# Performance work log

Hardware: AMD Instinct MI355X
Metric: run time of the kernel (lower is better)

The kernel has to match this reference:

```python
import jax, jax.numpy as jnp
import numpy as np

B, S, E = 4, 2048, 768
DFF = 4 * E
EPS = 1e-5


def _layernorm(x, g, b):
    mu = jnp.mean(x, axis=-1, keepdims=True)
    var = jnp.mean(jnp.square(x - mu), axis=-1, keepdims=True)
    return (x - mu) * jax.lax.rsqrt(var + EPS) * g + b


def setup_inputs() -> dict:
    key = jax.random.key(0)
    ks = jax.random.split(key, 16)
    w = lambda k, shp: jax.random.normal(k, shp, dtype=jnp.float32) * 0.02
    inp = {
        "x": jax.random.normal(ks[0], (B, S, E), dtype=jnp.float32),
        "kv": jax.random.normal(ks[1], (B, S, E), dtype=jnp.float32),
        "wq_w": w(ks[2], (E, E)), "wq_b": jnp.zeros((E,), jnp.float32),
        "wk_w": w(ks[3], (E, E)), "wk_b": jnp.zeros((E,), jnp.float32),
        "wv_w": w(ks[4], (E, E)), "wv_b": jnp.zeros((E,), jnp.float32),
        "ln1_g": jnp.ones((E,), jnp.float32), "ln1_b": jnp.zeros((E,), jnp.float32),
        "wq2_w": w(ks[5], (E, E)), "wq2_b": jnp.zeros((E,), jnp.float32),
        "wk2_w": w(ks[6], (E, E)), "wk2_b": jnp.zeros((E,), jnp.float32),
        "wv2_w": w(ks[7], (E, E)), "wv2_b": jnp.zeros((E,), jnp.float32),
        "ln2_g": jnp.ones((E,), jnp.float32), "ln2_b": jnp.zeros((E,), jnp.float32),
        "w1": w(ks[8], (DFF, E)), "b1": jnp.zeros((DFF,), jnp.float32),
        "w2": w(ks[9], (E, DFF)), "b2": jnp.zeros((E,), jnp.float32),
        "ln3_g": jnp.ones((E,), jnp.float32), "ln3_b": jnp.zeros((E,), jnp.float32),
    }
    return inp


def reference(x, kv, wq_w, wq_b, wk_w, wk_b, wv_w, wv_b, ln1_g, ln1_b,
              wq2_w, wq2_b, wk2_w, wk2_b, wv2_w, wv2_b, ln2_g, ln2_b,
              w1, b1, w2, b2, ln3_g, ln3_b):
    scalar = 1.0 / np.sqrt(E).astype(np.float32)
    mask_value = jnp.finfo(x.dtype).min
    s = x.shape[1]
    causal = jnp.triu(jnp.ones((s, s), dtype=bool), k=1)  # True above diagonal -> masked

    # ---- causal self-attention (single head, full E) ----
    q = x @ wq_w.T + wq_b
    k = x @ wk_w.T + wk_b
    v = x @ wv_w.T + wv_b
    scores = jnp.einsum('bqe,bke->bqk', q, k) * scalar
    scores = jnp.where(causal, mask_value, scores)
    h1 = jnp.einsum('bqk,bke->bqe', jax.nn.softmax(scores, axis=-1), v)
    x = _layernorm(x + h1, ln1_g, ln1_b)

    # ---- cross-attention over kv (no mask) ----
    q2 = x @ wq2_w.T + wq2_b
    k2 = kv @ wk2_w.T + wk2_b
    v2 = kv @ wv2_w.T + wv2_b
    scores2 = jnp.einsum('bqe,bke->bqk', q2, k2) * scalar
    h2 = jnp.einsum('bqk,bke->bqe', jax.nn.softmax(scores2, axis=-1), v2)
    x = _layernorm(x + h2, ln2_g, ln2_b)

    # ---- MLP: Linear -> ReLU -> Linear -> ReLU (note trailing ReLU) ----
    h = jax.nn.relu(x @ w1.T + b1)
    mlp = jax.nn.relu(h @ w2.T + b2)
    return _layernorm(x + mlp, ln3_g, ln3_b)
```

## Files before the change

kernel.cpp:

```cpp
#include <hip/hip_runtime.h>
#include <hip/hip_bf16.h>
#include <math.h>


typedef __bf16 bf16_t;
typedef bf16_t bf16x8 __attribute__((ext_vector_type(8)));
typedef float f32x4 __attribute__((ext_vector_type(4)));

struct MMDesc {
    const bf16_t* A;
    const bf16_t* B;
    const float* bias;
    __hip_bfloat16* C;
    float* lsum;
    int koff;
    int trans;
};
struct MMArgs { MMDesc g[8]; };

__device__ __forceinline__ void load16(const bf16_t* g, bf16_t* l) {
    __builtin_amdgcn_global_load_lds(
        (const __attribute__((address_space(1))) unsigned int*)g,
        (__attribute__((address_space(3))) unsigned int*)l, 16, 0, 0);
}

__device__ __forceinline__ void rd4(const bf16_t* p, int s0, int s1, bf16x8 f[4][2]) {
#pragma unroll
    for (int i = 0; i < 4; ++i) {
        f[i][0] = *(const bf16x8*)(p + i * 1024 + s0);
        f[i][1] = *(const bf16x8*)(p + i * 1024 + s1);
    }
}
__device__ __forceinline__ void rd2(const bf16_t* p, int s0, int s1, bf16x8 f[2][2]) {
#pragma unroll
    for (int i = 0; i < 2; ++i) {
        f[i][0] = *(const bf16x8*)(p + i * 1024 + s0);
        f[i][1] = *(const bf16x8*)(p + i * 1024 + s1);
    }
}

#define SBAR asm volatile("s_barrier" ::: "memory")
#define SCH  __builtin_amdgcn_sched_barrier(0)
#define MID  do { SCH; SBAR; SCH; __builtin_amdgcn_s_setprio(1); } while (0)
#define END0 do { __builtin_amdgcn_s_setprio(0); SCH; \
    asm volatile("s_waitcnt lgkmcnt(0)" ::: "memory"); SBAR; SCH; } while (0)
#define ENDV do { __builtin_amdgcn_s_setprio(0); SCH; \
    asm volatile("s_waitcnt vmcnt(4) lgkmcnt(0)" ::: "memory"); SBAR; SCH; } while (0)

#define QMFMA(mh, nh, BF) do { \
    _Pragma("unroll") \
    for (int ks = 0; ks < 2; ++ks) \
    _Pragma("unroll") \
    for (int mi = 0; mi < 4; ++mi) \
    _Pragma("unroll") \
    for (int ni = 0; ni < 2; ++ni) \
        acc[(mh) * 4 + mi][(nh) * 2 + ni] = __builtin_amdgcn_mfma_f32_16x16x32_bf16( \
            af[mi][ks], BF[ni][ks], acc[(mh) * 4 + mi][(nh) * 2 + ni], 0, 0, 0); \
} while (0)

__device__ __forceinline__ void mm8_core(
    const bf16_t* Ag, const bf16_t* Bg, int lda, int ldb, int K,
    bf16_t* lds, int w, int l, f32x4 acc[8][4])
{
    const long ldal = lda, ldbl = ldb;
    const int fr = l & 15, kq = l >> 4;
    const int rr = w * 8 + (l >> 3);
    const int c8e = ((l & 7) ^ (l >> 3)) * 8;
    const bf16_t* As = Ag + (long)rr * ldal + c8e;
    const bf16_t* Bs = Bg + (long)rr * ldbl + c8e;
    const int s0 = ((0 + kq) ^ (fr & 7)) * 8;
    const int s1 = ((4 + kq) ^ (fr & 7)) * 8;
    const bf16_t* lA = lds + ((w >> 2) * 64 + fr) * 64;
    const bf16_t* lB = lds + 16384 + ((w & 3) * 32 + fr) * 64;
    bf16_t* stA = lds + w * 512;
    bf16_t* stB = lds + 16384 + w * 512;

    auto stg = [&](int b, int isB, int h, int t) {
        const long ld = isB ? ldbl : ldal;
        const bf16_t* g = (isB ? Bs : As) + (long)h * 128 * ld + (long)t * 64;
        bf16_t* d = (isB ? stB : stA) + b * 32768 + h * 8192;
        load16(g, d);
        load16(g + 64 * ld, d + 4096);
    };

    bf16x8 af[4][2], bf0[2][2], bf1[2][2];
    const int NT = K >> 6, NI = NT >> 1;

    stg(0, 0, 0, 0); stg(0, 1, 0, 0); stg(0, 1, 1, 0); stg(0, 0, 1, 0);
    stg(1, 0, 0, 1); stg(1, 1, 0, 1);
    asm volatile("s_waitcnt vmcnt(4)" ::: "memory");
    SBAR; SCH;

    for (int i = 0; i < NI; ++i) {
        const int t1 = 2 * i + 1;
        int t2 = 2 * i + 2; if (t2 >= NT) t2 -= 2;
        int t3 = 2 * i + 3; if (t3 >= NT) t3 -= 2;
        rd4(lA, s0, s1, af); rd2(lB, s0, s1, bf0);
        stg(1, 1, 1, t1);
        MID; QMFMA(0, 0, bf0); END0;
        rd2(lB + 8192, s0, s1, bf1);
        stg(1, 0, 1, t1);
        MID; QMFMA(0, 1, bf1); END0;
        rd4(lA + 8192, s0, s1, af);
        stg(0, 0, 0, t2);
        MID; QMFMA(1, 0, bf0); END0;
        stg(0, 1, 0, t2);
        MID; QMFMA(1, 1, bf1); ENDV;
        rd4(lA + 32768, s0, s1, af); rd2(lB + 32768, s0, s1, bf0);
        stg(0, 1, 1, t2);
        MID; QMFMA(0, 0, bf0); END0;
        rd2(lB + 32768 + 8192, s0, s1, bf1);
        stg(0, 0, 1, t2);
        MID; QMFMA(0, 1, bf1); END0;
        rd4(lA + 32768 + 8192, s0, s1, af);
        stg(1, 0, 0, t3);
        MID; QMFMA(1, 0, bf0); END0;
        stg(1, 1, 0, t3);
        MID; QMFMA(1, 1, bf1); ENDV;
    }
    asm volatile("s_waitcnt vmcnt(0)" ::: "memory");
    SBAR; SCH;
}

template <bool RELU, bool CLAMPK>
__global__ __launch_bounds__(512, 2) void mm8_std(
    MMArgs args, int M, int N, int K, int lda, int ldb, float scale, int GX)
{
    __shared__ __align__(16) bf16_t lds[65536];
    const MMDesc dsc = args.g[blockIdx.z];

    const int lin = blockIdx.x;
    const int panel = lin / (8 * GX);
    const int rem = lin - panel * 8 * GX;
    const int bx = rem >> 3;
    const int by = panel * 8 + (rem & 7);
    const int m0 = by * 256, n0 = bx * 256;
    const int tid = threadIdx.x, w = tid >> 6, l = tid & 63;

    f32x4 acc[8][4];
    const f32x4 z4 = {0.f, 0.f, 0.f, 0.f};
#pragma unroll
    for (int i = 0; i < 8; ++i)
#pragma unroll
        for (int j = 0; j < 4; ++j) acc[i][j] = z4;

    int Keff = K;
    if (CLAMPK) {
        int km = (by + 1) * 256 - dsc.koff;
        Keff = km < K ? km : K;
    }
    if (!CLAMPK || Keff > 0)
        mm8_core(dsc.A + (long)m0 * lda, dsc.B + (long)n0 * ldb,
                 lda, ldb, Keff, lds, w, l, acc);

    const int fr = l & 15, erow = (l >> 4) * 4;
    const int wrow = (w >> 2) * 64, wcol = (w & 3) * 32;
    __hip_bfloat16* ct = (__hip_bfloat16*)lds;
#pragma unroll
    for (int mh = 0; mh < 2; ++mh) {
        if (mh) __syncthreads();
#pragma unroll
        for (int nh = 0; nh < 2; ++nh)
#pragma unroll
            for (int ni = 0; ni < 2; ++ni) {
                const int cl = nh * 128 + wcol + ni * 16 + fr;
                const float bv = dsc.bias ? dsc.bias[n0 + cl] : 0.f;
#pragma unroll
                for (int mi = 0; mi < 4; ++mi) {
                    const int lr = wrow + mi * 16 + erow;
                    const f32x4 a = acc[mh * 4 + mi][nh * 2 + ni];
#pragma unroll
                    for (int r = 0; r < 4; ++r) {
                        float v = a[r] * scale + bv;
                        if (RELU) v = fmaxf(v, 0.f);
                        ct[dsc.trans ? (cl * 136 + lr + r) : ((lr + r) * 264 + cl)]
                            = __float2bfloat16(v);
                    }
                }
            }
        __syncthreads();
        if (dsc.trans) {
            __hip_bfloat16* base = dsc.C + ((long)(m0 >> 11) * N + n0) * 2048
                                 + (m0 & 2047) + mh * 128;
#pragma unroll
            for (int u = 0; u < 8; ++u) {
                const int e = u * 4096 + tid * 8;
                *(uint4*)(base + (long)(e >> 7) * 2048 + (e & 127))
                    = *(const uint4*)(ct + (e >> 7) * 136 + (e & 127));
            }
        } else {
            __hip_bfloat16* base = dsc.C + (long)(m0 + mh * 128) * N + n0;
#pragma unroll
            for (int u = 0; u < 8; ++u) {
                const int e = u * 4096 + tid * 8;
                *(uint4*)(base + (long)(e >> 8) * N + (e & 255))
                    = *(const uint4*)(ct + (e >> 8) * 264 + (e & 255));
            }
        }
    }
}

template <bool CAUSAL>
__global__ __launch_bounds__(512, 2) void mm8_exp(
    MMArgs args, int N, int K, int lda, int ldb, float scale, int GX)
{
    __shared__ __align__(16) bf16_t lds[65536];
    const MMDesc dsc = args.g[blockIdx.z];

    int bx, by;
    if (CAUSAL) {
        const int t = blockIdx.x;
        by = (int)((sqrtf(8.f * t + 1.f) - 1.f) * 0.5f);
        while ((by + 1) * (by + 2) / 2 <= t) ++by;
        while (by * (by + 1) / 2 > t) --by;
        bx = t - by * (by + 1) / 2;
    } else {
        const int lin = blockIdx.x;
        const int panel = lin / (8 * GX);
        const int rem = lin - panel * 8 * GX;
        bx = rem >> 3;
        by = panel * 8 + (rem & 7);
    }
    const int m0 = by * 256, n0 = bx * 256;
    const int tid = threadIdx.x, w = tid >> 6, l = tid & 63;

    f32x4 acc[8][4];
    const f32x4 z4 = {0.f, 0.f, 0.f, 0.f};
#pragma unroll
    for (int i = 0; i < 8; ++i)
#pragma unroll
        for (int j = 0; j < 4; ++j) acc[i][j] = z4;

    mm8_core(dsc.A + (long)m0 * lda, dsc.B + (long)n0 * ldb,
             lda, ldb, K, lds, w, l, acc);

    const int fr = l & 15, erow = (l >> 4) * 4;
    const int wrow = (w >> 2) * 64, wcol = (w & 3) * 32;
    __hip_bfloat16* ct = (__hip_bfloat16*)lds;
#pragma unroll
    for (int mh = 0; mh < 2; ++mh) {
        if (mh) __syncthreads();
#pragma unroll
        for (int mi = 0; mi < 4; ++mi) {
            const int lr = wrow + mi * 16 + erow;
#pragma unroll
            for (int r = 0; r < 4; ++r) {
                const int grow = m0 + mh * 128 + lr + r;
                float rs = 0.f;
#pragma unroll
                for (int nh = 0; nh < 2; ++nh)
#pragma unroll
                    for (int ni = 0; ni < 2; ++ni) {
                        const int cl = nh * 128 + wcol + ni * 16 + fr;
                        float e;
                        if (CAUSAL && (n0 + cl) > grow)
                            e = 0.f;
                        else
                            e = __expf(acc[mh * 4 + mi][nh * 2 + ni][r] * scale);
                        ct[(lr + r) * 264 + cl] = __float2bfloat16(e);
                        rs += e;
                    }
#pragma unroll
                for (int o = 8; o > 0; o >>= 1) rs += __shfl_down(rs, o, 16);
                if ((l & 15) == 0) atomicAdd(&dsc.lsum[grow], rs);
            }
        }
        __syncthreads();
        __hip_bfloat16* base = dsc.C + (long)(m0 + mh * 128) * N + n0;
#pragma unroll
        for (int u = 0; u < 8; ++u) {
            const int e = u * 4096 + tid * 8;
            *(uint4*)(base + (long)(e >> 8) * N + (e & 255))
                = *(const uint4*)(ct + (e >> 8) * 264 + (e & 255));
        }
    }
}

__device__ __forceinline__ float waveReduceSum(float v) {
#pragma unroll
    for (int o = 32; o > 0; o >>= 1) v += __shfl_down(v, o, 64);
    return v;
}
__device__ __forceinline__ float blockReduceSum(float v, float* s) {
    int lane = threadIdx.x & 63, w = threadIdx.x >> 6;
    v = waveReduceSum(v);
    __syncthreads();
    if (lane == 0) s[w] = v;
    __syncthreads();
    return s[0] + s[1] + s[2] + s[3];
}

template <bool BR, bool XF32>
__global__ __launch_bounds__(256) void ln_kernel(
    const float* __restrict__ xf, const __hip_bfloat16* __restrict__ xh,
    const __hip_bfloat16* __restrict__ h1, const __hip_bfloat16* __restrict__ h2,
    const float* __restrict__ hbias, const float* __restrict__ lsum,
    const float* __restrict__ g, const float* __restrict__ beta,
    float* __restrict__ outf, __hip_bfloat16* __restrict__ outb) {
    __shared__ float red[4];
    const int E = 768;
    const long row = blockIdx.x;
    const float hscale = lsum ? (1.f / lsum[row]) : 1.f;

    float vals[3];
    float sum = 0.f;
#pragma unroll
    for (int i = 0; i < 3; ++i) {
        int c = threadIdx.x + i * 256;
        float t = __bfloat162float(h1[row * E + c]) + __bfloat162float(h2[row * E + c]);
        if (BR) t = fmaxf(t + hbias[c], 0.f);
        else t *= hscale;
        float xv = XF32 ? xf[row * E + c] : __bfloat162float(xh[row * E + c]);
        vals[i] = xv + t;
        sum += vals[i];
    }
    sum = blockReduceSum(sum, red);
    const float mean = sum * (1.f / 768.f);

    float ss = 0.f;
#pragma unroll
    for (int i = 0; i < 3; ++i) {
        float d = vals[i] - mean;
        ss += d * d;
    }
    ss = blockReduceSum(ss, red);
    const float inv = rsqrtf(ss * (1.f / 768.f) + 1e-5f);

#pragma unroll
    for (int i = 0; i < 3; ++i) {
        int c = threadIdx.x + i * 256;
        float v = (vals[i] - mean) * inv * g[c] + beta[c];
        if (outf) outf[row * E + c] = v;
        if (outb) outb[row * E + c] = __float2bfloat16(v);
    }
}

struct CvtPtrs {
    const float* s[10];
    __hip_bfloat16* d[10];
};
__global__ __launch_bounds__(256) void cvt_all(CvtPtrs p) {
    int bid = blockIdx.x, seg, off;
    if (bid < 3456) {
        seg = bid / 576;
        off = (bid % 576) * 1024;
    } else if (bid < 8064) {
        int t = bid - 3456;
        seg = 6 + t / 2304;
        off = (t % 2304) * 1024;
    } else {
        int t = bid - 8064;
        seg = 8 + t / 6144;
        off = (t % 6144) * 1024;
    }
    const float* s = p.s[seg];
    __hip_bfloat16* d = p.d[seg];
    int i = off + threadIdx.x * 4;
    float4 v = *(const float4*)(s + i);
    d[i + 0] = __float2bfloat16(v.x);
    d[i + 1] = __float2bfloat16(v.y);
    d[i + 2] = __float2bfloat16(v.z);
    d[i + 3] = __float2bfloat16(v.w);
}

extern "C" void kernel_launch(void* const* d_in, const int* in_sizes, int n_in,
                              void* d_out, int out_size, void* d_ws, size_t ws_size,
                              hipStream_t stream) {
    const int Bb = 4, S = 2048, E = 768, DFF = 3072;
    const int Nr = Bb * S;

    const float* x    = (const float*)d_in[0];
    const float* kv   = (const float*)d_in[1];
    const float* wq_w = (const float*)d_in[2];
    const float* wq_b = (const float*)d_in[3];
    const float* wk_w = (const float*)d_in[4];
    const float* wk_b = (const float*)d_in[5];
    const float* wv_w = (const float*)d_in[6];
    const float* wv_b = (const float*)d_in[7];
    const float* ln1g = (const float*)d_in[8];
    const float* ln1b = (const float*)d_in[9];
    const float* wq2w = (const float*)d_in[10];
    const float* wq2b = (const float*)d_in[11];
    const float* wk2w = (const float*)d_in[12];
    const float* wk2b = (const float*)d_in[13];
    const float* wv2w = (const float*)d_in[14];
    const float* wv2b = (const float*)d_in[15];
    const float* ln2g = (const float*)d_in[16];
    const float* ln2b = (const float*)d_in[17];
    const float* w1   = (const float*)d_in[18];
    const float* b1   = (const float*)d_in[19];
    const float* w2   = (const float*)d_in[20];
    const float* b2   = (const float*)d_in[21];
    const float* ln3g = (const float*)d_in[22];
    const float* ln3b = (const float*)d_in[23];
    float* out = (float*)d_out;

    char* wsp = (char*)d_ws;
    auto alloc = [&](size_t bytes) {
        char* p = wsp;
        wsp += (bytes + 255) & ~(size_t)255;
        return p;
    };
    const size_t nSE = (size_t)Nr * E;
    const size_t nSS = (size_t)Bb * S * S;
    __hip_bfloat16* Pb   = (__hip_bfloat16*)alloc(nSS * 2);
    __hip_bfloat16* qb   = (__hip_bfloat16*)alloc(nSE * 2);
    __hip_bfloat16* kb   = (__hip_bfloat16*)alloc(nSE * 2);
    __hip_bfloat16* hffb = Pb;
    __hip_bfloat16* vtb  = (__hip_bfloat16*)alloc(nSE * 2);
    __hip_bfloat16* xb   = (__hip_bfloat16*)alloc(nSE * 2);
    __hip_bfloat16* kvb  = (__hip_bfloat16*)alloc(nSE * 2);
    __hip_bfloat16* actb = (__hip_bfloat16*)alloc(nSE * 2);
    __hip_bfloat16* hA   = (__hip_bfloat16*)alloc(nSE * 2);
    __hip_bfloat16* hB   = (__hip_bfloat16*)alloc(nSE * 2);
    __hip_bfloat16* wqb   = (__hip_bfloat16*)alloc((size_t)E * E * 2);
    __hip_bfloat16* wkb   = (__hip_bfloat16*)alloc((size_t)E * E * 2);
    __hip_bfloat16* wvb   = (__hip_bfloat16*)alloc((size_t)E * E * 2);
    __hip_bfloat16* wq2bm = (__hip_bfloat16*)alloc((size_t)E * E * 2);
    __hip_bfloat16* wk2bm = (__hip_bfloat16*)alloc((size_t)E * E * 2);
    __hip_bfloat16* wv2bm = (__hip_bfloat16*)alloc((size_t)E * E * 2);
    __hip_bfloat16* w1b   = (__hip_bfloat16*)alloc((size_t)DFF * E * 2);
    __hip_bfloat16* w2b   = (__hip_bfloat16*)alloc((size_t)E * DFF * 2);
    float* lsum1 = (float*)alloc((size_t)Nr * 4);
    float* lsum2 = (float*)alloc((size_t)Nr * 4);

    const float scale = 1.0f / sqrtf((float)E);
    const dim3 blk(256);
    const dim3 blk5(512);

    hipMemsetAsync(lsum1, 0, (size_t)Nr * 4 * 2, stream);

    CvtPtrs cp;
    cp.s[0] = wq_w; cp.d[0] = wqb;
    cp.s[1] = wk_w; cp.d[1] = wkb;
    cp.s[2] = wv_w; cp.d[2] = wvb;
    cp.s[3] = wq2w; cp.d[3] = wq2bm;
    cp.s[4] = wk2w; cp.d[4] = wk2bm;
    cp.s[5] = wv2w; cp.d[5] = wv2bm;
    cp.s[6] = w1;   cp.d[6] = w1b;
    cp.s[7] = w2;   cp.d[7] = w2b;
    cp.s[8] = x;    cp.d[8] = xb;
    cp.s[9] = kv;   cp.d[9] = kvb;
    cvt_all<<<8064 + 12288, blk, 0, stream>>>(cp);

    {
        MMArgs a{};
        a.g[0] = {(const bf16_t*)xb, (const bf16_t*)wqb, wq_b, qb, nullptr, 0, 0};
        a.g[1] = {(const bf16_t*)xb, (const bf16_t*)wkb, wk_b, kb, nullptr, 0, 0};
        a.g[2] = {(const bf16_t*)xb, (const bf16_t*)wvb, wv_b, vtb, nullptr, 0, 1};
        mm8_std<false, false><<<dim3(96, 1, 3), blk5, 0, stream>>>(
            a, Nr, E, E, E, E, 1.f, 3);
    }
    {
        MMArgs a{};
        for (int b = 0; b < 4; ++b)
            a.g[b] = {(const bf16_t*)qb + (long)b * S * E,
                      (const bf16_t*)kb + (long)b * S * E, nullptr,
                      Pb + (long)b * S * S, lsum1 + b * S, 0, 0};
        mm8_exp<true><<<dim3(36, 1, 4), blk5, 0, stream>>>(a, S, E, E, E, scale, 8);
    }
    {
        MMArgs a{};
        for (int b = 0; b < 4; ++b)
            for (int ks = 0; ks < 2; ++ks)
                a.g[b * 2 + ks] = {(const bf16_t*)Pb + (long)b * S * S + ks * 1024,
                                   (const bf16_t*)vtb + (long)b * E * S + ks * 1024,
                                   nullptr, (ks ? hB : hA) + (long)b * S * E,
                                   nullptr, ks * 1024, 0};
        mm8_std<false, true><<<dim3(24, 1, 8), blk5, 0, stream>>>(
            a, S, E, 1024, S, S, 1.f, 3);
    }
    ln_kernel<false, true><<<Nr, blk, 0, stream>>>(
        x, nullptr, hA, hB, nullptr, lsum1, ln1g, ln1b, nullptr, actb);

    {
        MMArgs a{};
        a.g[0] = {(const bf16_t*)actb, (const bf16_t*)wq2bm, wq2b, qb, nullptr, 0, 0};
        a.g[1] = {(const bf16_t*)kvb, (const bf16_t*)wk2bm, wk2b, kb, nullptr, 0, 0};
        a.g[2] = {(const bf16_t*)kvb, (const bf16_t*)wv2bm, wv2b, vtb, nullptr, 0, 1};
        mm8_std<false, false><<<dim3(96, 1, 3), blk5, 0, stream>>>(
            a, Nr, E, E, E, E, 1.f, 3);
    }
    {
        MMArgs a{};
        for (int b = 0; b < 4; ++b)
            a.g[b] = {(const bf16_t*)qb + (long)b * S * E,
                      (const bf16_t*)kb + (long)b * S * E, nullptr,
                      Pb + (long)b * S * S, lsum2 + b * S, 0, 0};
        mm8_exp<false><<<dim3(64, 1, 4), blk5, 0, stream>>>(a, S, E, E, E, scale, 8);
    }
    {
        MMArgs a{};
        for (int b = 0; b < 4; ++b)
            for (int ks = 0; ks < 2; ++ks)
                a.g[b * 2 + ks] = {(const bf16_t*)Pb + (long)b * S * S + ks * 1024,
                                   (const bf16_t*)vtb + (long)b * E * S + ks * 1024,
                                   nullptr, (ks ? hB : hA) + (long)b * S * E,
                                   nullptr, 0, 0};
        mm8_std<false, false><<<dim3(24, 1, 8), blk5, 0, stream>>>(
            a, S, E, 1024, S, S, 1.f, 3);
    }
    ln_kernel<false, false><<<Nr, blk, 0, stream>>>(
        nullptr, actb, hA, hB, nullptr, lsum2, ln2g, ln2b, nullptr, actb);

    {
        MMArgs a{};
        a.g[0] = {(const bf16_t*)actb, (const bf16_t*)w1b, b1, hffb, nullptr, 0, 0};
        mm8_std<true, false><<<dim3(384, 1, 1), blk5, 0, stream>>>(
            a, Nr, DFF, E, E, E, 1.f, 12);
    }
    {
        MMArgs a{};
        a.g[0] = {(const bf16_t*)hffb, (const bf16_t*)w2b, nullptr, hA, nullptr, 0, 0};
        a.g[1] = {(const bf16_t*)hffb + 1536, (const bf16_t*)w2b + 1536, nullptr,
                  hB, nullptr, 0, 0};
        mm8_std<false, false><<<dim3(96, 1, 2), blk5, 0, stream>>>(
            a, Nr, E, 1536, DFF, DFF, 1.f, 3);
    }
    ln_kernel<true, false><<<Nr, blk, 0, stream>>>(
        nullptr, actb, hA, hB, b2, nullptr, ln3g, ln3b, out, nullptr);
}
```

Baseline: 542.7 us.

## Hoist cross-attn K/V projections into first projection launch and relax GEMM waits

The cross-attention K2/V2 projections depend only on kv, so they move into the first batched projection launch (z=5), and the later launch computes only Q2. This fills the GPU better and removes work from the serial chain. K2/V2 are staged in the output buffer as scratch, which is safe only if d_out is large enough and is overwritten afterwards. Separately, the GEMM main loop drops the per-phase lgkmcnt(0) wait plus trailing barrier, keeping a single barrier before each MFMA block and an explicit vmcnt(4) wait. This relies on the remaining barriers and the compiler's own waits to keep LDS reads correct.

```diff
diff --git a/kernel.cpp b/kernel.cpp
--- a/kernel.cpp
+++ b/kernel.cpp
@@ -41,11 +41,10 @@
 
 #define SBAR asm volatile("s_barrier" ::: "memory")
 #define SCH  __builtin_amdgcn_sched_barrier(0)
-#define MID  do { SCH; SBAR; SCH; __builtin_amdgcn_s_setprio(1); } while (0)
-#define END0 do { __builtin_amdgcn_s_setprio(0); SCH; \
-    asm volatile("s_waitcnt lgkmcnt(0)" ::: "memory"); SBAR; SCH; } while (0)
-#define ENDV do { __builtin_amdgcn_s_setprio(0); SCH; \
-    asm volatile("s_waitcnt vmcnt(4) lgkmcnt(0)" ::: "memory"); SBAR; SCH; } while (0)
+#define PBAR do { SCH; SBAR; SCH; } while (0)
+#define PRIO1 __builtin_amdgcn_s_setprio(1)
+#define PRIO0 __builtin_amdgcn_s_setprio(0)
+#define VMC4 asm volatile("s_waitcnt vmcnt(4)" ::: "memory")
 
 #define QMFMA(mh, nh, BF) do { \
     _Pragma("unroll") \
@@ -97,26 +96,28 @@
         int t3 = 2 * i + 3; if (t3 >= NT) t3 -= 2;
         rd4(lA, s0, s1, af); rd2(lB, s0, s1, bf0);
         stg(1, 1, 1, t1);
-        MID; QMFMA(0, 0, bf0); END0;
+        PBAR; PRIO1; QMFMA(0, 0, bf0); PRIO0;
         rd2(lB + 8192, s0, s1, bf1);
         stg(1, 0, 1, t1);
-        MID; QMFMA(0, 1, bf1); END0;
+        PBAR; PRIO1; QMFMA(0, 1, bf1); PRIO0;
         rd4(lA + 8192, s0, s1, af);
         stg(0, 0, 0, t2);
-        MID; QMFMA(1, 0, bf0); END0;
+        PBAR; PRIO1; QMFMA(1, 0, bf0); PRIO0;
         stg(0, 1, 0, t2);
-        MID; QMFMA(1, 1, bf1); ENDV;
+        VMC4;
+        PBAR; PRIO1; QMFMA(1, 1, bf1); PRIO0;
         rd4(lA + 32768, s0, s1, af); rd2(lB + 32768, s0, s1, bf0);
         stg(0, 1, 1, t2);
-        MID; QMFMA(0, 0, bf0); END0;
+        PBAR; PRIO1; QMFMA(0, 0, bf0); PRIO0;
         rd2(lB + 32768 + 8192, s0, s1, bf1);
         stg(0, 0, 1, t2);
-        MID; QMFMA(0, 1, bf1); END0;
+        PBAR; PRIO1; QMFMA(0, 1, bf1); PRIO0;
         rd4(lA + 32768 + 8192, s0, s1, af);
         stg(1, 0, 0, t3);
-        MID; QMFMA(1, 0, bf0); END0;
+        PBAR; PRIO1; QMFMA(1, 0, bf0); PRIO0;
         stg(1, 1, 0, t3);
-        MID; QMFMA(1, 1, bf1); ENDV;
+        VMC4;
+        PBAR; PRIO1; QMFMA(1, 1, bf1); PRIO0;
     }
     asm volatile("s_waitcnt vmcnt(0)" ::: "memory");
     SBAR; SCH;
@@ -424,6 +425,9 @@
     float* lsum1 = (float*)alloc((size_t)Nr * 4);
     float* lsum2 = (float*)alloc((size_t)Nr * 4);
 
+    __hip_bfloat16* k2b  = (__hip_bfloat16*)d_out;
+    __hip_bfloat16* vtb2 = k2b + nSE;
+
     const float scale = 1.0f / sqrtf((float)E);
     const dim3 blk(256);
     const dim3 blk5(512);
@@ -445,10 +449,12 @@
 
     {
         MMArgs a{};
-        a.g[0] = {(const bf16_t*)xb, (const bf16_t*)wqb, wq_b, qb, nullptr, 0, 0};
-        a.g[1] = {(const bf16_t*)xb, (const bf16_t*)wkb, wk_b, kb, nullptr, 0, 0};
-        a.g[2] = {(const bf16_t*)xb, (const bf16_t*)wvb, wv_b, vtb, nullptr, 0, 1};
-        mm8_std<false, false><<<dim3(96, 1, 3), blk5, 0, stream>>>(
+        a.g[0] = {(const bf16_t*)xb,  (const bf16_t*)wqb,   wq_b, qb,   nullptr, 0, 0};
+        a.g[1] = {(const bf16_t*)xb,  (const bf16_t*)wkb,   wk_b, kb,   nullptr, 0, 0};
+        a.g[2] = {(const bf16_t*)xb,  (const bf16_t*)wvb,   wv_b, vtb,  nullptr, 0, 1};
+        a.g[3] = {(const bf16_t*)kvb, (const bf16_t*)wk2bm, wk2b, k2b,  nullptr, 0, 0};
+        a.g[4] = {(const bf16_t*)kvb, (const bf16_t*)wv2bm, wv2b, vtb2, nullptr, 0, 1};
+        mm8_std<false, false><<<dim3(96, 1, 5), blk5, 0, stream>>>(
             a, Nr, E, E, E, E, 1.f, 3);
     }
     {
@@ -476,16 +482,14 @@
     {
         MMArgs a{};
         a.g[0] = {(const bf16_t*)actb, (const bf16_t*)wq2bm, wq2b, qb, nullptr, 0, 0};
-        a.g[1] = {(const bf16_t*)kvb, (const bf16_t*)wk2bm, wk2b, kb, nullptr, 0, 0};
-        a.g[2] = {(const bf16_t*)kvb, (const bf16_t*)wv2bm, wv2b, vtb, nullptr, 0, 1};
-        mm8_std<false, false><<<dim3(96, 1, 3), blk5, 0, stream>>>(
+        mm8_std<false, false><<<dim3(96, 1, 1), blk5, 0, stream>>>(
             a, Nr, E, E, E, E, 1.f, 3);
     }
     {
         MMArgs a{};
         for (int b = 0; b < 4; ++b)
             a.g[b] = {(const bf16_t*)qb + (long)b * S * E,
-                      (const bf16_t*)kb + (long)b * S * E, nullptr,
+                      (const bf16_t*)k2b + (long)b * S * E, nullptr,
                       Pb + (long)b * S * S, lsum2 + b * S, 0, 0};
         mm8_exp<false><<<dim3(64, 1, 4), blk5, 0, stream>>>(a, S, E, E, E, scale, 8);
     }
@@ -494,7 +498,7 @@
         for (int b = 0; b < 4; ++b)
             for (int ks = 0; ks < 2; ++ks)
                 a.g[b * 2 + ks] = {(const bf16_t*)Pb + (long)b * S * S + ks * 1024,
-                                   (const bf16_t*)vtb + (long)b * E * S + ks * 1024,
+                                   (const bf16_t*)vtb2 + (long)b * E * S + ks * 1024,
                                    nullptr, (ks ? hB : hA) + (long)b * S * E,
                                    nullptr, 0, 0};
         mm8_std<false, false><<<dim3(24, 1, 8), blk5, 0, stream>>>(
```

Result: faster. 496.1 us (-8.6%).
